# Kernel tuning notes

Hardware: AMD Instinct MI355X
Metric: run time of the kernel (lower is better)

Reference implementation:

```python
import jax, jax.numpy as jnp
import numpy as np

N_HEAD = 12
D_HEAD = 64  # inner_dim 768 / 12 heads

def quick_gelu(x):
    return x * jax.nn.sigmoid(1.702 * x)

def setup_inputs() -> dict:
    key = jax.random.key(0)
    ks = jax.random.split(key, 12)
    B, Nv, Lt, Cv, Ct, Ci = 256, 196, 32, 768, 512, 768
    s = lambda k, shp, fan: jax.random.normal(k, shp, jnp.float32) / np.sqrt(fan)
    return {
        "vis_tokens": jax.random.normal(ks[0], (B, Nv, Cv), jnp.float32),
        "text_tokens": jax.random.normal(ks[1], (B, Lt, Ct), jnp.float32),
        "Wq": s(ks[2], (Cv, Ci), Cv), "bq": jnp.zeros((Ci,), jnp.float32),
        "Wk": s(ks[3], (Ct, Ci), Ct), "bk": jnp.zeros((Ci,), jnp.float32),
        "Wv": s(ks[4], (Ct, Ci), Ct), "bv": jnp.zeros((Ci,), jnp.float32),
        "W1": s(ks[5], (Ci, Ci), Ci), "b1": jnp.zeros((Ci,), jnp.float32),
        "W2": s(ks[6], (Ci, 2), Ci), "b2": jnp.zeros((2,), jnp.float32),
    }

def reference(vis_tokens, text_tokens, Wq, bq, Wk, bk, Wv, bv, W1, b1, W2, b2):
    B, Nv, _ = vis_tokens.shape
    Lt = text_tokens.shape[1]
    Ci = Wq.shape[1]
    # projections -> [B, H, N, D]
    q = (vis_tokens @ Wq + bq).reshape(B, Nv, N_HEAD, D_HEAD).transpose(0, 2, 1, 3)
    k = (text_tokens @ Wk + bk).reshape(B, Lt, N_HEAD, D_HEAD).transpose(0, 2, 1, 3)
    v = (text_tokens @ Wv + bv).reshape(B, Lt, N_HEAD, D_HEAD).transpose(0, 2, 1, 3)
    scores = jnp.einsum('bhnd,bhld->bhnl', q, k) / np.sqrt(D_HEAD).astype(np.float32)
    attn = jax.nn.softmax(scores, axis=-1)           # [B,H,Nv,Lt]
    ctx = jnp.einsum('bhnl,bhld->bhnd', attn, v)      # [B,H,Nv,D]
    ctx = ctx.transpose(0, 2, 1, 3).reshape(B, Nv, Ci)
    fused = ctx + vis_tokens[..., :Ci]
    logits = quick_gelu(fused @ W1 + b1) @ W2 + b2    # [B,Nv,2]
    rel_BN = attn.mean(axis=-1).mean(axis=1)          # [B,Nv]
    return (logits, rel_BN)
```

## Files before the change

kernel.cpp:

```cpp
#include <hip/hip_runtime.h>
#include <hip/hip_bf16.h>


typedef __attribute__((ext_vector_type(8))) short bf16x8;
typedef __attribute__((ext_vector_type(4))) float f32x4;

__device__ __forceinline__ float bf2f(unsigned short u) {
    return __uint_as_float(((unsigned int)u) << 16);
}
__device__ __forceinline__ unsigned short f2bf(float f) {
    unsigned int x = __float_as_uint(f);
    unsigned int r = (x + 0x7FFFu + ((x >> 16) & 1u)) >> 16;
    return (unsigned short)r;
}

#define GLOAD_LDS16(gp, lp)                                                    \
    __builtin_amdgcn_global_load_lds(                                          \
        (__attribute__((address_space(1))) void*)(gp),                         \
        (__attribute__((address_space(3))) void*)(lp), 16, 0, 0)

#define BAR()  __builtin_amdgcn_s_barrier()
#define LGKM0 asm volatile("s_waitcnt lgkmcnt(0)" ::: "memory")
#define VMC0  asm volatile("s_waitcnt vmcnt(0)" ::: "memory")
#define VMC4  asm volatile("s_waitcnt vmcnt(4)" ::: "memory")
#define VMC6  asm volatile("s_waitcnt vmcnt(6)" ::: "memory")

__global__ void cvt_bf16_kernel(const float* __restrict__ in,
                                unsigned short* __restrict__ out, int n4) {
    int i = blockIdx.x * 256 + threadIdx.x;
    if (i >= n4) return;
    float4 v = ((const float4*)in)[i];
    ushort4 o;
    o.x = f2bf(v.x); o.y = f2bf(v.y); o.z = f2bf(v.z); o.w = f2bf(v.w);
    ((ushort4*)out)[i] = o;
}

__global__ void transpose_cvt_kernel(const float* __restrict__ W,
                                     unsigned short* __restrict__ Wt,
                                     int K, int N) {
    __shared__ float tile[32][33];
    int n0 = blockIdx.x * 32, k0 = blockIdx.y * 32;
    int tx = threadIdx.x & 31, ty = threadIdx.x >> 5;
    #pragma unroll
    for (int r = ty; r < 32; r += 8)
        tile[r][tx] = W[(size_t)(k0 + r) * N + n0 + tx];
    __syncthreads();
    #pragma unroll
    for (int r = ty; r < 32; r += 8)
        Wt[(size_t)(n0 + r) * K + k0 + tx] = f2bf(tile[tx][r]);
}

template<int KTOT, int GELU>
__global__ __launch_bounds__(512, 1)
void gemm256_kernel(const unsigned short* __restrict__ A,
                    const unsigned short* __restrict__ Bt,
                    const float* __restrict__ bias,
                    unsigned short* __restrict__ C) {
    constexpr int NT = KTOT / 64;
    constexpr int GS = 520;
    constexpr int TSZ = 32 * GS;
    __shared__ unsigned short As[2 * TSZ];
    __shared__ unsigned short Bs[2 * TSZ];
    const int tid = threadIdx.x;
    const int lane = tid & 63, wave = tid >> 6;
    const int wm = wave >> 2, wn = wave & 3;
    const int lr = lane & 15, quad = lane >> 4;
    const int s7 = lane & 7;
    const int rp = ((lr >> 3) * GS) + ((lane & 7) << 6);

    const int nwg = gridDim.x;
    const int qq = nwg >> 3, r8 = nwg & 7;
    const int xcd = blockIdx.x & 7, loc = blockIdx.x >> 3;
    const int wg = (xcd < r8 ? xcd * (qq + 1) : r8 * (qq + 1) + (xcd - r8) * qq) + loc;
    const int mt = wg / 3, nt = wg - mt * 3;
    const size_t m0 = (size_t)mt * 256;
    const int n0 = nt * 256;

    const int swz = ((lane & 7) ^ (lane >> 3)) * 8;
    const unsigned short* gA = A + (m0 + (lane >> 3)) * (size_t)KTOT + swz;
    const unsigned short* gB = Bt + ((size_t)(n0 + (lane >> 3))) * KTOT + swz;

#define STG_A(b, t, h) do {                                                    \
    const int g0_ = (h) * 16 + wave * 2;                                       \
    GLOAD_LDS16(gA + (size_t)(g0_) * 8 * KTOT + (t) * 64,                      \
                As + (b) * TSZ + (g0_) * GS);                                  \
    GLOAD_LDS16(gA + (size_t)(g0_ + 1) * 8 * KTOT + (t) * 64,                  \
                As + (b) * TSZ + (g0_ + 1) * GS);                              \
} while (0)
#define STG_B(b, t, h) do {                                                    \
    const int g0_ = (h) * 16 + wave * 2;                                       \
    GLOAD_LDS16(gB + (size_t)(g0_) * 8 * KTOT + (t) * 64,                      \
                Bs + (b) * TSZ + (g0_) * GS);                                  \
    GLOAD_LDS16(gB + (size_t)(g0_ + 1) * 8 * KTOT + (t) * 64,                  \
                Bs + (b) * TSZ + (g0_ + 1) * GS);                              \
} while (0)

    f32x4 acc[8][4] = {};
    bf16x8 aR[4][2], bR[4][2];

#define LDA_FRAGS(ibase)                                                       \
    _Pragma("unroll")                                                          \
    for (int i = 0; i < 4; ++i)                                                \
        _Pragma("unroll")                                                      \
        for (int kk = 0; kk < 2; ++kk)                                         \
            aR[i][kk] = *(const bf16x8*)(pa + (wm * 16 + ((ibase) + i) * 2) * GS \
                         + rp + ((((kk * 4) + quad) ^ s7) << 3));

#define LDB_FRAGS(jbase)                                                       \
    _Pragma("unroll")                                                          \
    for (int j = 0; j < 2; ++j)                                                \
        _Pragma("unroll")                                                      \
        for (int kk = 0; kk < 2; ++kk)                                         \
            bR[(jbase) + j][kk] = *(const bf16x8*)(pb + (wn * 8 + ((jbase) + j) * 2) * GS \
                         + rp + ((((kk * 4) + quad) ^ s7) << 3));

#define MFMA_Q(I0, J0)                                                         \
    __builtin_amdgcn_s_setprio(1);                                             \
    _Pragma("unroll")                                                          \
    for (int i = 0; i < 4; ++i)                                                \
        _Pragma("unroll")                                                      \
        for (int j = 0; j < 2; ++j)                                            \
            _Pragma("unroll")                                                  \
            for (int kk = 0; kk < 2; ++kk)                                     \
                acc[(I0) + i][(J0) + j] = __builtin_amdgcn_mfma_f32_16x16x32_bf16( \
                    aR[i][kk], bR[(J0) + j][kk], acc[(I0) + i][(J0) + j], 0, 0, 0); \
    __builtin_amdgcn_s_setprio(0);

    STG_B(0, 0, 0); STG_B(0, 0, 1); STG_A(0, 0, 0); STG_A(0, 0, 1);
    VMC4;
    STG_B(1, 1, 0); STG_B(1, 1, 1); STG_A(1, 1, 0);
    VMC6;
    BAR();

    for (int t = 0; t < NT - 1; ++t) {
        const int buf = t & 1;
        const unsigned short* pa = As + buf * TSZ;
        const unsigned short* pb = Bs + buf * TSZ;
        const bool last = (t == NT - 2);
        LDA_FRAGS(0); LDB_FRAGS(0);
        STG_A(buf ^ 1, t + 1, 1);
        BAR(); LGKM0;
        MFMA_Q(0, 0);
        BAR();
        LDB_FRAGS(2);
        BAR(); LGKM0;
        MFMA_Q(0, 2);
        BAR();
        LDA_FRAGS(4);
        if (!last) { STG_B(buf, t + 2, 0); } else { VMC4; }
        BAR(); LGKM0;
        MFMA_Q(4, 0);
        BAR();
        if (!last) { STG_B(buf, t + 2, 1); STG_A(buf, t + 2, 0); VMC6; }
        else { VMC0; }
        BAR(); LGKM0;
        MFMA_Q(4, 2);
        BAR();
    }
    {
        const unsigned short* pa = As + ((NT - 1) & 1) * TSZ;
        const unsigned short* pb = Bs + ((NT - 1) & 1) * TSZ;
        LDA_FRAGS(0); LDB_FRAGS(0); LDB_FRAGS(2);
        MFMA_Q(0, 0);
        MFMA_Q(0, 2);
        LDA_FRAGS(4);
        MFMA_Q(4, 0);
        MFMA_Q(4, 2);
    }

    #pragma unroll
    for (int j = 0; j < 4; ++j) {
        int col = n0 + wn * 64 + j * 16 + lr;
        float bv = bias[col];
        #pragma unroll
        for (int i = 0; i < 8; ++i) {
            #pragma unroll
            for (int r2 = 0; r2 < 4; ++r2) {
                size_t row = m0 + wm * 128 + i * 16 + quad * 4 + r2;
                float x = acc[i][j][r2] + bv;
                if (GELU) x = x / (1.0f + __expf(-1.702f * x));
                C[row * 768 + col] = f2bf(x);
            }
        }
    }
#undef STG_A
#undef STG_B
#undef LDA_FRAGS
#undef LDB_FRAGS
#undef MFMA_Q
}

template<int KTOT, int GELU, int MTILES>
__global__ __launch_bounds__(256, 2)
void gemm_bt_kernel(const unsigned short* __restrict__ A,
                    const unsigned short* __restrict__ Bt,
                    const float* __restrict__ bias,
                    unsigned short* __restrict__ C) {
    constexpr int GS = 520;
    __shared__ unsigned short As[16 * GS];
    __shared__ unsigned short Bs[16 * GS];
    const int tid = threadIdx.x;
    const int lane = tid & 63, wave = tid >> 6;
    const int id = blockIdx.x;
    const int xcd = id & 7, local = id >> 3;
    const int nt = local % 6, mt = xcd * (MTILES / 8) + local / 6;
    const size_t m0 = (size_t)mt * 128;
    const int n0 = nt * 128;
    const int wm = (wave >> 1) * 64, wn = (wave & 1) * 64;
    const int lr = lane & 15, quad = lane >> 4;

    const int swz = ((lane & 7) ^ (lane >> 3)) * 8;
    const unsigned short* gA = A + (m0 + wave * 32 + (lane >> 3)) * KTOT + swz;
    const unsigned short* gB = Bt + ((size_t)n0 + wave * 32 + (lane >> 3)) * KTOT + swz;
    unsigned short* lA = As + (wave * 4) * GS;
    unsigned short* lB = Bs + (wave * 4) * GS;

    f32x4 acc[4][4] = {};

    for (int kt = 0; kt < KTOT; kt += 64) {
        #pragma unroll
        for (int i = 0; i < 4; ++i) {
            GLOAD_LDS16(gA + (size_t)i * 8 * KTOT + kt, lA + i * GS);
            GLOAD_LDS16(gB + (size_t)i * 8 * KTOT + kt, lB + i * GS);
        }
        __syncthreads();
        #pragma unroll
        for (int kk = 0; kk < 64; kk += 32) {
            bf16x8 fa[4], fb[4];
            #pragma unroll
            for (int i = 0; i < 4; ++i) {
                int r = wm + i * 16 + lr;
                int g = (kk >> 3) + quad;
                fa[i] = *(const bf16x8*)(As + (r >> 3) * GS + (r & 7) * 64 +
                                         ((g ^ (r & 7)) << 3));
            }
            #pragma unroll
            for (int j = 0; j < 4; ++j) {
                int r = wn + j * 16 + lr;
                int g = (kk >> 3) + quad;
                fb[j] = *(const bf16x8*)(Bs + (r >> 3) * GS + (r & 7) * 64 +
                                         ((g ^ (r & 7)) << 3));
            }
            #pragma unroll
            for (int i = 0; i < 4; ++i)
                #pragma unroll
                for (int j = 0; j < 4; ++j)
                    acc[i][j] = __builtin_amdgcn_mfma_f32_16x16x32_bf16(
                        fa[i], fb[j], acc[i][j], 0, 0, 0);
        }
        __syncthreads();
    }

    #pragma unroll
    for (int j = 0; j < 4; ++j) {
        int col = n0 + wn + j * 16 + lr;
        float bv = bias[col];
        #pragma unroll
        for (int i = 0; i < 4; ++i) {
            #pragma unroll
            for (int r = 0; r < 4; ++r) {
                size_t row = m0 + wm + i * 16 + quad * 4 + r;
                float x = acc[i][j][r] + bv;
                if (GELU) x = x / (1.0f + __expf(-1.702f * x));
                C[row * 768 + col] = f2bf(x);
            }
        }
    }
}

__global__ __launch_bounds__(256, 4)
void attn_mfma_kernel(const unsigned short* __restrict__ Q,
                      const unsigned short* __restrict__ Kb,
                      const unsigned short* __restrict__ Vb,
                      unsigned short* __restrict__ RF) {
    constexpr int KS = 72;
    constexpr int VS = 34;
    constexpr int PS = 40;
    constexpr int CS = 72;
    __shared__ unsigned short Ks[32 * KS];
    __shared__ unsigned short Vt[64 * VS];
    __shared__ unsigned short Pb[4][16 * PS];
    __shared__ unsigned short Cb[4][16 * CS];
    const int tid = threadIdx.x;
    const int b = blockIdx.x / 12, h = blockIdx.x % 12;
    const int lane = tid & 63, wave = tid >> 6;
    const int lr = lane & 15, quad = lane >> 4;

    {
        int l = tid >> 3, d8 = (tid & 7) * 8;
        size_t base = ((size_t)b * 32 + l) * 768 + (size_t)h * 64 + d8;
        bf16x8 kv = *(const bf16x8*)(Kb + base);
        bf16x8 vv = *(const bf16x8*)(Vb + base);
        *(bf16x8*)(Ks + l * KS + d8) = kv;
        #pragma unroll
        for (int j = 0; j < 8; ++j)
            Vt[(d8 + j) * VS + l] = (unsigned short)vv[j];
    }
    __syncthreads();

    bf16x8 fbK[2][2];
    #pragma unroll
    for (int n = 0; n < 2; ++n)
        #pragma unroll
        for (int ks = 0; ks < 2; ++ks)
            fbK[n][ks] = *(const bf16x8*)(Ks + (n * 16 + lr) * KS + ks * 32 + quad * 8);
    bf16x8 fbV[4];
    #pragma unroll
    for (int d = 0; d < 4; ++d)
        fbV[d] = *(const bf16x8*)(Vt + (d * 16 + lr) * VS + quad * 8);

    const size_t qbase = (size_t)b * 196 * 768 + (size_t)h * 64;

    for (int t = wave; t < 13; t += 4) {
        const int m0 = t * 16;
        int qrow = m0 + lr; if (qrow > 195) qrow = 195;
        const unsigned short* qp = Q + qbase + (size_t)qrow * 768;
        bf16x8 fa0 = *(const bf16x8*)(qp + quad * 8);
        bf16x8 fa1 = *(const bf16x8*)(qp + 32 + quad * 8);
        f32x4 s0 = {}, s1 = {};
        s0 = __builtin_amdgcn_mfma_f32_16x16x32_bf16(fa0, fbK[0][0], s0, 0, 0, 0);
        s0 = __builtin_amdgcn_mfma_f32_16x16x32_bf16(fa1, fbK[0][1], s0, 0, 0, 0);
        s1 = __builtin_amdgcn_mfma_f32_16x16x32_bf16(fa0, fbK[1][0], s1, 0, 0, 0);
        s1 = __builtin_amdgcn_mfma_f32_16x16x32_bf16(fa1, fbK[1][1], s1, 0, 0, 0);

        float p0[4], p1[4], m4[4], s4[4];
        #pragma unroll
        for (int r = 0; r < 4; ++r) {
            p0[r] = s0[r] * 0.125f;
            p1[r] = s1[r] * 0.125f;
            m4[r] = fmaxf(p0[r], p1[r]);
        }
        #pragma unroll
        for (int off = 1; off < 16; off <<= 1)
            #pragma unroll
            for (int r = 0; r < 4; ++r)
                m4[r] = fmaxf(m4[r], __shfl_xor(m4[r], off));
        #pragma unroll
        for (int r = 0; r < 4; ++r) {
            p0[r] = __expf(p0[r] - m4[r]);
            p1[r] = __expf(p1[r] - m4[r]);
            s4[r] = p0[r] + p1[r];
        }
        #pragma unroll
        for (int off = 1; off < 16; off <<= 1)
            #pragma unroll
            for (int r = 0; r < 4; ++r)
                s4[r] += __shfl_xor(s4[r], off);
        #pragma unroll
        for (int r = 0; r < 4; ++r) {
            float inv = __builtin_amdgcn_rcpf(s4[r]);
            unsigned short* pr = &Pb[wave][(quad * 4 + r) * PS];
            pr[lr]      = f2bf(p0[r] * inv);
            pr[16 + lr] = f2bf(p1[r] * inv);
        }

        bf16x8 fap = *(const bf16x8*)(&Pb[wave][lr * PS + quad * 8]);
        f32x4 c[4];
        #pragma unroll
        for (int d = 0; d < 4; ++d) {
            f32x4 z = {};
            c[d] = __builtin_amdgcn_mfma_f32_16x16x32_bf16(fap, fbV[d], z, 0, 0, 0);
        }
        #pragma unroll
        for (int d = 0; d < 4; ++d)
            #pragma unroll
            for (int r = 0; r < 4; ++r)
                Cb[wave][(quad * 4 + r) * CS + d * 16 + lr] = f2bf(c[d][r]);
        #pragma unroll
        for (int i = 0; i < 2; ++i) {
            int c2 = lane + i * 64;
            int row = c2 >> 3, col8 = (c2 & 7) * 8;
            int grow = m0 + row;
            if (grow < 196) {
                bf16x8 cv = *(const bf16x8*)(&Cb[wave][row * CS + col8]);
                unsigned short* gp = RF + qbase + (size_t)grow * 768 + col8;
                bf16x8 rv = *(const bf16x8*)gp;
                bf16x8 ov;
                #pragma unroll
                for (int j = 0; j < 8; ++j)
                    ov[j] = (short)f2bf(bf2f((unsigned short)cv[j]) +
                                        bf2f((unsigned short)rv[j]));
                *(bf16x8*)gp = ov;
            }
        }
    }
}

__global__ __launch_bounds__(256)
void mlp2_kernel(const unsigned short* __restrict__ Hb,
                 const float* __restrict__ W2,
                 const float* __restrict__ b2,
                 float* __restrict__ out) {
    __shared__ float w2s[2][768];
    const int tid = threadIdx.x;
    for (int i = tid; i < 1536; i += 256) w2s[i & 1][i >> 1] = W2[i];
    __syncthreads();
    const int sub = tid & 7;
    const int r = tid >> 3;
    const size_t row = (size_t)blockIdx.x * 32 + r;
    float a0 = 0.f, a1 = 0.f;
    #pragma unroll
    for (int i = 0; i < 12; ++i) {
        int base = i * 64 + sub * 8;
        bf16x8 hv = *(const bf16x8*)(Hb + row * 768 + base);
        #pragma unroll
        for (int j = 0; j < 8; ++j) {
            float hf = bf2f((unsigned short)hv[j]);
            a0 += hf * w2s[0][base + j];
            a1 += hf * w2s[1][base + j];
        }
    }
    #pragma unroll
    for (int o = 4; o >= 1; o >>= 1) {
        a0 += __shfl_down(a0, o, 8);
        a1 += __shfl_down(a1, o, 8);
    }
    if (sub == 0) {
        out[row * 2]      = a0 + b2[0];
        out[row * 2 + 1]  = a1 + b2[1];
        out[100352 + row] = 0.03125f;
    }
}

extern "C" void kernel_launch(void* const* d_in, const int* in_sizes, int n_in,
                              void* d_out, int out_size, void* d_ws, size_t ws_size,
                              hipStream_t stream) {
    const float* vis = (const float*)d_in[0];
    const float* txt = (const float*)d_in[1];
    const float* Wq  = (const float*)d_in[2];
    const float* bq  = (const float*)d_in[3];
    const float* Wk  = (const float*)d_in[4];
    const float* bk  = (const float*)d_in[5];
    const float* Wv  = (const float*)d_in[6];
    const float* bv  = (const float*)d_in[7];
    const float* W1  = (const float*)d_in[8];
    const float* b1  = (const float*)d_in[9];
    const float* W2  = (const float*)d_in[10];
    const float* b2  = (const float*)d_in[11];
    float* out = (float*)d_out;

    char* w = (char*)d_ws;
    unsigned short* Abf = (unsigned short*)(w);
    unsigned short* Tbf = (unsigned short*)(w + 77070336);
    unsigned short* Wqt = (unsigned short*)(w + 85458944);
    unsigned short* Wkt = (unsigned short*)(w + 86638592);
    unsigned short* Wvt = (unsigned short*)(w + 87425024);
    unsigned short* W1t = (unsigned short*)(w + 88211456);
    unsigned short* Qbf = (unsigned short*)(w + 89391104);
    unsigned short* Kbf = (unsigned short*)(w + 166461440);
    unsigned short* Vbf = (unsigned short*)(w + 179044352);
    unsigned short* Hbf = Qbf;

    cvt_bf16_kernel<<<37632, 256, 0, stream>>>(vis, Abf, 9633792);
    cvt_bf16_kernel<<<4096, 256, 0, stream>>>(txt, Tbf, 1048576);
    transpose_cvt_kernel<<<dim3(24, 24), 256, 0, stream>>>(Wq, Wqt, 768, 768);
    transpose_cvt_kernel<<<dim3(24, 16), 256, 0, stream>>>(Wk, Wkt, 512, 768);
    transpose_cvt_kernel<<<dim3(24, 16), 256, 0, stream>>>(Wv, Wvt, 512, 768);
    transpose_cvt_kernel<<<dim3(24, 24), 256, 0, stream>>>(W1, W1t, 768, 768);

    gemm256_kernel<768, 0><<<588, 512, 0, stream>>>(Abf, Wqt, bq, Qbf);
    gemm_bt_kernel<512, 0, 64><<<384, 256, 0, stream>>>(Tbf, Wkt, bk, Kbf);
    gemm_bt_kernel<512, 0, 64><<<384, 256, 0, stream>>>(Tbf, Wvt, bv, Vbf);

    attn_mfma_kernel<<<3072, 256, 0, stream>>>(Qbf, Kbf, Vbf, Abf);

    gemm256_kernel<768, 1><<<588, 512, 0, stream>>>(Abf, W1t, b1, Hbf);

    mlp2_kernel<<<1568, 256, 0, stream>>>(Hbf, W2, b2, out);
}
```

Baseline: 560.3 us.

## Restructure GEMM LDS tiles into k-split panels with XOR slot swizzle

Changes the shared-memory layout of the 256x256 GEMM tiles from padded rows with a per-lane XOR swizzle to two 32-wide k panels of 32-element rows. The global-to-LDS staging addresses and the fragment reads change to match, and a smaller XOR on the 8-element slot replaces the padding. The goal is to cut LDS bank conflicts and address arithmetic on fragment loads. The epilogue is also reordered so bias values are loaded once and stores walk columns for each row. The risk is a mismatch between the staging layout and the read layout, or new bank conflicts.

```diff
diff --git a/kernel.cpp b/kernel.cpp
--- a/kernel.cpp
+++ b/kernel.cpp
@@ -57,16 +57,14 @@
                     const float* __restrict__ bias,
                     unsigned short* __restrict__ C) {
     constexpr int NT = KTOT / 64;
-    constexpr int GS = 520;
-    constexpr int TSZ = 32 * GS;
+    constexpr int PAN = 8192;
+    constexpr int TSZ = 2 * PAN;
     __shared__ unsigned short As[2 * TSZ];
     __shared__ unsigned short Bs[2 * TSZ];
     const int tid = threadIdx.x;
     const int lane = tid & 63, wave = tid >> 6;
     const int wm = wave >> 2, wn = wave & 3;
     const int lr = lane & 15, quad = lane >> 4;
-    const int s7 = lane & 7;
-    const int rp = ((lr >> 3) * GS) + ((lane & 7) << 6);
 
     const int nwg = gridDim.x;
     const int qq = nwg >> 3, r8 = nwg & 7;
@@ -76,23 +74,29 @@
     const size_t m0 = (size_t)mt * 256;
     const int n0 = nt * 256;
 
-    const int swz = ((lane & 7) ^ (lane >> 3)) * 8;
-    const unsigned short* gA = A + (m0 + (lane >> 3)) * (size_t)KTOT + swz;
-    const unsigned short* gB = Bt + ((size_t)(n0 + (lane >> 3))) * KTOT + swz;
+    const int slotoff = ((quad ^ (((lr >> 3) & 1) << 1)) << 3);
+    const int aBase = (wm * 128 + lr) * 32 + slotoff;
+    const int bBase = (wn * 64 + lr) * 32 + slotoff;
+
+    const int sg = (lane & 3) ^ (((lane >> 5) & 1) << 1);
+    const unsigned short* gA = A + (m0 + (lane >> 2)) * (size_t)KTOT + sg * 8;
+    const unsigned short* gB = Bt + ((size_t)(n0 + (lane >> 2))) * KTOT + sg * 8;
+    const int sp = wave >> 2;
+    const int sr = (wave & 3) * 32;
 
 #define STG_A(b, t, h) do {                                                    \
-    const int g0_ = (h) * 16 + wave * 2;                                       \
-    GLOAD_LDS16(gA + (size_t)(g0_) * 8 * KTOT + (t) * 64,                      \
-                As + (b) * TSZ + (g0_) * GS);                                  \
-    GLOAD_LDS16(gA + (size_t)(g0_ + 1) * 8 * KTOT + (t) * 64,                  \
-                As + (b) * TSZ + (g0_ + 1) * GS);                              \
+    const int r0_ = (h) * 128 + sr;                                            \
+    GLOAD_LDS16(gA + (size_t)r0_ * KTOT + (t) * 64 + sp * 32,                  \
+                As + (b) * TSZ + sp * PAN + r0_ * 32);                         \
+    GLOAD_LDS16(gA + (size_t)(r0_ + 16) * KTOT + (t) * 64 + sp * 32,           \
+                As + (b) * TSZ + sp * PAN + (r0_ + 16) * 32);                  \
 } while (0)
 #define STG_B(b, t, h) do {                                                    \
-    const int g0_ = (h) * 16 + wave * 2;                                       \
-    GLOAD_LDS16(gB + (size_t)(g0_) * 8 * KTOT + (t) * 64,                      \
-                Bs + (b) * TSZ + (g0_) * GS);                                  \
-    GLOAD_LDS16(gB + (size_t)(g0_ + 1) * 8 * KTOT + (t) * 64,                  \
-                Bs + (b) * TSZ + (g0_ + 1) * GS);                              \
+    const int r0_ = (h) * 128 + sr;                                            \
+    GLOAD_LDS16(gB + (size_t)r0_ * KTOT + (t) * 64 + sp * 32,                  \
+                Bs + (b) * TSZ + sp * PAN + r0_ * 32);                         \
+    GLOAD_LDS16(gB + (size_t)(r0_ + 16) * KTOT + (t) * 64 + sp * 32,           \
+                Bs + (b) * TSZ + sp * PAN + (r0_ + 16) * 32);                  \
 } while (0)
 
     f32x4 acc[8][4] = {};
@@ -103,16 +107,14 @@
     for (int i = 0; i < 4; ++i)                                                \
         _Pragma("unroll")                                                      \
         for (int kk = 0; kk < 2; ++kk)                                         \
-            aR[i][kk] = *(const bf16x8*)(pa + (wm * 16 + ((ibase) + i) * 2) * GS \
-                         + rp + ((((kk * 4) + quad) ^ s7) << 3));
+            aR[i][kk] = *(const bf16x8*)(pa + kk * PAN + aBase + ((ibase) + i) * 512);
 
 #define LDB_FRAGS(jbase)                                                       \
     _Pragma("unroll")                                                          \
     for (int j = 0; j < 2; ++j)                                                \
         _Pragma("unroll")                                                      \
         for (int kk = 0; kk < 2; ++kk)                                         \
-            bR[(jbase) + j][kk] = *(const bf16x8*)(pb + (wn * 8 + ((jbase) + j) * 2) * GS \
-                         + rp + ((((kk * 4) + quad) ^ s7) << 3));
+            bR[(jbase) + j][kk] = *(const bf16x8*)(pb + kk * PAN + bBase + ((jbase) + j) * 512);
 
 #define MFMA_Q(I0, J0)                                                         \
     __builtin_amdgcn_s_setprio(1);                                             \
@@ -168,18 +170,21 @@
         MFMA_Q(4, 2);
     }
 
-    #pragma unroll
-    for (int j = 0; j < 4; ++j) {
-        int col = n0 + wn * 64 + j * 16 + lr;
-        float bv = bias[col];
-        #pragma unroll
-        for (int i = 0; i < 8; ++i) {
-            #pragma unroll
-            for (int r2 = 0; r2 < 4; ++r2) {
-                size_t row = m0 + wm * 128 + i * 16 + quad * 4 + r2;
-                float x = acc[i][j][r2] + bv;
+    float bvv[4];
+    #pragma unroll
+    for (int j = 0; j < 4; ++j)
+        bvv[j] = bias[n0 + wn * 64 + j * 16 + lr];
+    #pragma unroll
+    for (int i = 0; i < 8; ++i) {
+        #pragma unroll
+        for (int r2 = 0; r2 < 4; ++r2) {
+            size_t row = m0 + wm * 128 + i * 16 + quad * 4 + r2;
+            unsigned short* cp = C + row * 768 + n0 + wn * 64 + lr;
+            #pragma unroll
+            for (int j = 0; j < 4; ++j) {
+                float x = acc[i][j][r2] + bvv[j];
                 if (GELU) x = x / (1.0f + __expf(-1.702f * x));
-                C[row * 768 + col] = f2bf(x);
+                cp[j * 16] = f2bf(x);
             }
         }
     }
```

Result: faster. 545.9 us (-2.6%).
